# Optimization experiments

Hardware: AMD Instinct MI355X
Metric: run time of the kernel (lower is better)

## Reference

```python
import jax, jax.numpy as jnp
import numpy as np

BS, N, D, H = 4, 128, 768, 8
HD = D // H
FFN = 3072
E = BS * N * N
NORM_FACTOR = 100.0
NORM_CONST = 1.0
EPS_LN = 1e-5


def _ln(v, s, b):
    m = jnp.mean(v, -1, keepdims=True)
    var = jnp.mean(jnp.square(v - m), -1, keepdims=True)
    return (v - m) * jax.lax.rsqrt(var + EPS_LN) * s + b


def _glu(v, w, b):
    a, g = jnp.split(v @ w.T + b, 2, axis=-1)
    return a * jnp.square(jax.nn.relu(g))  # GLU with ReLU^2 gate activation


def setup_inputs() -> dict:
    key = jax.random.key(0)
    ks = jax.random.split(key, 24)
    rn = lambda i, shape, s=1.0: jax.random.normal(ks[i], shape, jnp.float32) * s
    # fully-connected per-graph edge_index with block structure
    base = jnp.arange(BS, dtype=jnp.int32) * N
    ii = jnp.repeat(jnp.arange(N, dtype=jnp.int32), N)
    jj = jnp.tile(jnp.arange(N, dtype=jnp.int32), N)
    row = (base[:, None] + ii[None, :]).reshape(-1)
    col = (base[:, None] + jj[None, :]).reshape(-1)
    edge_index = jnp.stack([row, col], 0)  # [2, E]
    return {
        'h': rn(0, (BS * N, D)),
        'x': rn(1, (BS * N, 3)),
        'edge_attr': rn(2, (E, 1)),
        'node_mask': jnp.ones((BS * N, 1), jnp.float32),
        'edge_mask': jnp.ones((E, 1), jnp.float32),
        'linker_mask': jnp.ones((BS * N, 1), jnp.float32),
        'in_proj_w': rn(3, (3 * D, D), 0.02), 'in_proj_b': jnp.zeros((3 * D,)),
        'out_proj_w': rn(4, (D, D), 0.02), 'out_proj_b': jnp.zeros((D,)),
        'ln1_s': jnp.ones((D,)), 'ln1_b': jnp.zeros((D,)),
        'ln2_s': jnp.ones((D,)), 'ln2_b': jnp.zeros((D,)),
        'fc1_w': rn(5, (2 * FFN, D), 0.02), 'fc1_b': jnp.zeros((2 * FFN,)),
        'fc2_w': rn(6, (2 * D, FFN), 0.02), 'fc2_b': jnp.zeros((2 * D,)),
        'efc1_w': rn(7, (H, 2), 0.5), 'efc1_b': jnp.zeros((H,)),
        'efc2_w': rn(8, (H, 2), 0.5), 'efc2_b': jnp.zeros((H,)),
        'cm1_w': rn(9, (D, 2 * D + 2), 0.02), 'cm1_b': jnp.zeros((D,)),
        'cm2_w': rn(10, (D, D), 0.02), 'cm2_b': jnp.zeros((D,)),
        'cm3_w': rn(11, (1, D), 0.001),
        'edge_index': edge_index,
    }


def _forward(h, x, edge_attr, node_mask, edge_mask, linker_mask,
             in_proj_w, in_proj_b, out_proj_w, out_proj_b,
             ln1_s, ln1_b, ln2_s, ln2_b, fc1_w, fc1_b, fc2_w, fc2_b,
             efc1_w, efc1_b, efc2_w, efc2_b,
             cm1_w, cm1_b, cm2_w, cm2_b, cm3_w, edge_index):
    row, col = edge_index[0], edge_index[1]
    # coord2diff
    diff = x[row] - x[col]                                   # [E,3]
    radial = jnp.sum(jnp.square(diff), 1, keepdims=True)     # [E,1]
    coord_diff = diff / (jnp.sqrt(radial + 1e-8) + NORM_CONST)
    ea = jnp.concatenate([radial, edge_attr], 1)             # [E,2]

    def edge_to_heads(w, b):
        y = (ea @ w.T + b) * edge_mask                       # [E,H]
        return jnp.transpose(y.reshape(BS, N, N, H), (0, 3, 1, 2))  # [BS,H,N,N]

    attn_bias = edge_to_heads(efc1_w, efc1_b)
    gw = edge_to_heads(efc2_w, efc2_b)

    # Graphormer3DEncoderLayer (eval mode: dropout = identity)
    hb = h.reshape(BS, N, D)
    hn = _ln(hb, ln1_s, ln1_b)
    q, k, v = jnp.split(hn @ in_proj_w.T + in_proj_b, 3, axis=-1)
    q = q.reshape(BS, N, H, HD) * (HD ** -0.5)
    k = k.reshape(BS, N, H, HD)
    v = v.reshape(BS, N, H, HD)
    scores = jnp.einsum('bihd,bjhd->bhij', q, k) + attn_bias
    probs = jnp.tanh(gw) * jax.nn.softmax(scores, axis=-1)   # tanh-gated softmax
    att = jnp.einsum('bhij,bjhd->bihd', probs, v).reshape(BS, N, D)
    h1 = hb + (att @ out_proj_w.T + out_proj_b)
    ff = _ln(h1, ln2_s, ln2_b)
    ff = jax.nn.gelu(_glu(ff, fc1_w, fc1_b), approximate=False)
    ff = _glu(ff, fc2_w, fc2_b)
    h_out = (h1 + ff).reshape(BS * N, D) * node_mask

    # EquivariantUpdate (tanh=False branch)
    ei = jnp.concatenate([h_out[row], h_out[col], ea], 1)    # [E, 2D+2]
    t = jax.nn.silu(ei @ cm1_w.T + cm1_b)
    t = jax.nn.silu(t @ cm2_w.T + cm2_b)
    s = t @ cm3_w.T                                          # [E,1]
    trans = coord_diff * s * edge_mask
    agg = jax.ops.segment_sum(trans, row, num_segments=BS * N) / NORM_FACTOR
    x_out = (x + agg * linker_mask) * node_mask
    return h_out, x_out


def reference(h, x, edge_attr, node_mask, edge_mask, linker_mask,
              in_proj_w, in_proj_b, out_proj_w, out_proj_b,
              ln1_s, ln1_b, ln2_s, ln2_b, fc1_w, fc1_b, fc2_w, fc2_b,
              efc1_w, efc1_b, efc2_w, efc2_b,
              cm1_w, cm1_b, cm2_w, cm2_b, cm3_w, edge_index):
    return _forward(h, x, edge_attr, node_mask, edge_mask, linker_mask,
                    in_proj_w, in_proj_b, out_proj_w, out_proj_b,
                    ln1_s, ln1_b, ln2_s, ln2_b, fc1_w, fc1_b, fc2_w, fc2_b,
                    efc1_w, efc1_b, efc2_w, efc2_b,
                    cm1_w, cm1_b, cm2_w, cm2_b, cm3_w, edge_index)
```

## Files before the change

### kernel.cpp

```cpp
#include <hip/hip_runtime.h>
#include <cstdint>
#include <cstddef>

#define BSZ   4
#define NN    128
#define DD    768
#define HH    8
#define HD    96
#define FFN   3072
#define NNODE (BSZ*NN)
#define NE    (NNODE*NN)

typedef unsigned short u16;
typedef __bf16 bf16x8 __attribute__((ext_vector_type(8)));
typedef float  f32x4  __attribute__((ext_vector_type(4)));
typedef unsigned short u16x8 __attribute__((ext_vector_type(8)));
typedef unsigned short u16x4 __attribute__((ext_vector_type(4)));
typedef unsigned short u16x2 __attribute__((ext_vector_type(2)));

__device__ __forceinline__ float bf2f(u16 a){
    unsigned u = ((unsigned)a) << 16; float f; __builtin_memcpy(&f, &u, 4); return f;
}
__device__ __forceinline__ u16 f2bf(float f){
    unsigned u; __builtin_memcpy(&u, &f, 4);
    u = (u + 0x7fffu + ((u >> 16) & 1u)) >> 16;
    return (u16)u;
}
__device__ __forceinline__ f32x4 mfma16(bf16x8 a, bf16x8 b, f32x4 c){
    return __builtin_amdgcn_mfma_f32_16x16x32_bf16(a, b, c, 0, 0, 0);
}
__device__ __forceinline__ bf16x8 frag(const u16* p){
    u16x8 v = *(const u16x8*)p; return __builtin_bit_cast(bf16x8, v);
}
__device__ __forceinline__ void gload16(const void* g, void* l){
    __builtin_amdgcn_global_load_lds((const __attribute__((address_space(1))) void*)g,
                                     (__attribute__((address_space(3))) void*)l, 16, 0, 0);
}
__device__ __forceinline__ float fsilu(float f){
    return f * __builtin_amdgcn_rcpf(1.f + __expf(-f));
}
__device__ __forceinline__ float wred_sum(float v){
    #pragma unroll
    for (int m = 1; m < 64; m <<= 1) v += __shfl_xor(v, m);
    return v;
}
__device__ __forceinline__ float wred_max(float v){
    #pragma unroll
    for (int m = 1; m < 64; m <<= 1) v = fmaxf(v, __shfl_xor(v, m));
    return v;
}

__global__ __launch_bounds__(256) void ln_k(const float* __restrict__ in,
                                            const float* __restrict__ sc,
                                            const float* __restrict__ bi,
                                            u16* __restrict__ out){
    int row = blockIdx.x, tid = threadIdx.x;
    const float* r = in + (size_t)row * DD;
    float x0 = r[tid], x1 = r[tid + 256], x2 = r[tid + 512];
    float s = x0 + x1 + x2, q = x0*x0 + x1*x1 + x2*x2;
    s = wred_sum(s); q = wred_sum(q);
    __shared__ float rs[4], rq[4];
    int w = tid >> 6;
    if ((tid & 63) == 0){ rs[w] = s; rq[w] = q; }
    __syncthreads();
    float ts = rs[0] + rs[1] + rs[2] + rs[3];
    float tq = rq[0] + rq[1] + rq[2] + rq[3];
    float mean = ts * (1.f / DD);
    float var  = tq * (1.f / DD) - mean * mean;
    float rstd = rsqrtf(var + 1e-5f);
    u16* o = out + (size_t)row * DD;
    o[tid]       = f2bf((x0 - mean) * rstd * sc[tid]       + bi[tid]);
    o[tid + 256] = f2bf((x1 - mean) * rstd * sc[tid + 256] + bi[tid + 256]);
    o[tid + 512] = f2bf((x2 - mean) * rstd * sc[tid + 512] + bi[tid + 512]);
}

__device__ __forceinline__ void stage64(u16* __restrict__ dst, const u16* __restrict__ src,
                                        int ld, int kk, int tid){
    #pragma unroll
    for (int p = 0; p < 2; p++){
        int idx = p * 256 + tid;
        int row = idx >> 3, ch = idx & 7;
        int sch = ch ^ (row & 7);
        gload16(src + (size_t)row * ld + kk + sch * 8, dst + idx * 8);
    }
}

__device__ __forceinline__ void stageA(u16* __restrict__ As, const u16* __restrict__ A,
                                       int m0, int lda, int kk, int tid){
    #pragma unroll
    for (int p = 0; p < 2; p++){
        int idx = p * 256 + tid;
        int row = idx >> 3, ch = idx & 7;
        *(uint4*)&As[row * 72 + ch * 8] = *(const uint4*)(A + (size_t)(m0 + row) * lda + kk + ch * 8);
    }
}
__device__ __forceinline__ void stageBf32(u16* __restrict__ Bs, const float* __restrict__ B,
                                          int n0, int ldb, int kk, int tid){
    #pragma unroll
    for (int p = 0; p < 4; p++){
        int idx = p * 256 + tid;
        int row = idx >> 4, c4 = idx & 15;
        float4 v = *(const float4*)(B + (size_t)(n0 + row) * ldb + kk + c4 * 4);
        u16x4 o; o[0] = f2bf(v.x); o[1] = f2bf(v.y); o[2] = f2bf(v.z); o[3] = f2bf(v.w);
        *(u16x4*)&Bs[row * 72 + c4 * 4] = o;
    }
}

#define GEMM_PRO(AB, BB)                                                            \
    const int tid = threadIdx.x;                                                    \
    const int m0 = blockIdx.y * 64, n0 = blockIdx.x * 64;                           \
    const int w = tid >> 6, lane = tid & 63, quad = lane >> 4, l15 = lane & 15;     \
    const int wy = w >> 1, wx = w & 1;                                              \
    const int swz = (l15 & 7) << 4;                                                 \
    const u16* Abase = AB; const u16* Bbase = BB;

__global__ __launch_bounds__(256) void gemm_bt2(const u16* __restrict__ A, int lda,
                                                const u16* __restrict__ B, int ldb,
                                                const float* __restrict__ bias,
                                                u16* __restrict__ C, int ldc, int K){
    __shared__ u16 As[2][64 * 64];
    __shared__ u16 Bs[2][64 * 64];
    GEMM_PRO(A + (size_t)m0 * lda, B + (size_t)n0 * ldb)
    f32x4 acc[2][2];
    #pragma unroll
    for (int i = 0; i < 2; i++)
        #pragma unroll
        for (int j = 0; j < 2; j++){ f32x4 z = {0.f,0.f,0.f,0.f}; acc[i][j] = z; }

    stage64(As[0], Abase, lda, 0, tid);
    stage64(Bs[0], Bbase, ldb, 0, tid);
    __syncthreads();
    const int NS = K / 64;
    #pragma unroll 1
    for (int s = 0; s < NS; s++){
        const int cur = s & 1;
        if (s + 1 < NS){
            stage64(As[cur ^ 1], Abase, lda, (s + 1) * 64, tid);
            stage64(Bs[cur ^ 1], Bbase, ldb, (s + 1) * 64, tid);
        }
        const char* ab = (const char*)&As[cur][0];
        const char* bb = (const char*)&Bs[cur][0];
        #pragma unroll
        for (int k0 = 0; k0 < 64; k0 += 32){
            const int kbx = ((k0 + quad * 8) * 2) ^ swz;
            bf16x8 a0 = frag((const u16*)(ab + (wy * 32 + l15) * 128 + kbx));
            bf16x8 a1 = frag((const u16*)(ab + (wy * 32 + 16 + l15) * 128 + kbx));
            bf16x8 b0 = frag((const u16*)(bb + (wx * 32 + l15) * 128 + kbx));
            bf16x8 b1 = frag((const u16*)(bb + (wx * 32 + 16 + l15) * 128 + kbx));
            acc[0][0] = mfma16(a0, b0, acc[0][0]);
            acc[0][1] = mfma16(a0, b1, acc[0][1]);
            acc[1][0] = mfma16(a1, b0, acc[1][0]);
            acc[1][1] = mfma16(a1, b1, acc[1][1]);
        }
        __syncthreads();
    }
    #pragma unroll
    for (int j = 0; j < 2; j++){
        int n = n0 + wx * 32 + j * 16 + l15;
        float bv = bias[n];
        #pragma unroll
        for (int i = 0; i < 2; i++){
            #pragma unroll
            for (int r = 0; r < 4; r++){
                int m = m0 + wy * 32 + i * 16 + quad * 4 + r;
                C[(size_t)m * ldc + n] = f2bf(acc[i][j][r] + bv);
            }
        }
    }
}

__global__ __launch_bounds__(256) void gemm_proj2(const u16* __restrict__ A,
                                                  const u16* __restrict__ B,
                                                  const float* __restrict__ bias,
                                                  const float* __restrict__ h,
                                                  float* __restrict__ h1f){
    __shared__ u16 As[2][64 * 64];
    __shared__ u16 Bs[2][64 * 64];
    GEMM_PRO(A + (size_t)m0 * DD, B + (size_t)n0 * DD)
    f32x4 acc[2][2];
    #pragma unroll
    for (int i = 0; i < 2; i++)
        #pragma unroll
        for (int j = 0; j < 2; j++){ f32x4 z = {0.f,0.f,0.f,0.f}; acc[i][j] = z; }

    stage64(As[0], Abase, DD, 0, tid);
    stage64(Bs[0], Bbase, DD, 0, tid);
    __syncthreads();
    #pragma unroll 1
    for (int s = 0; s < 12; s++){
        const int cur = s & 1;
        if (s + 1 < 12){
            stage64(As[cur ^ 1], Abase, DD, (s + 1) * 64, tid);
            stage64(Bs[cur ^ 1], Bbase, DD, (s + 1) * 64, tid);
        }
        const char* ab = (const char*)&As[cur][0];
        const char* bb = (const char*)&Bs[cur][0];
        #pragma unroll
        for (int k0 = 0; k0 < 64; k0 += 32){
            const int kbx = ((k0 + quad * 8) * 2) ^ swz;
            bf16x8 a0 = frag((const u16*)(ab + (wy * 32 + l15) * 128 + kbx));
            bf16x8 a1 = frag((const u16*)(ab + (wy * 32 + 16 + l15) * 128 + kbx));
            bf16x8 b0 = frag((const u16*)(bb + (wx * 32 + l15) * 128 + kbx));
            bf16x8 b1 = frag((const u16*)(bb + (wx * 32 + 16 + l15) * 128 + kbx));
            acc[0][0] = mfma16(a0, b0, acc[0][0]);
            acc[0][1] = mfma16(a0, b1, acc[0][1]);
            acc[1][0] = mfma16(a1, b0, acc[1][0]);
            acc[1][1] = mfma16(a1, b1, acc[1][1]);
        }
        __syncthreads();
    }
    #pragma unroll
    for (int j = 0; j < 2; j++){
        int n = n0 + wx * 32 + j * 16 + l15;
        float bv = bias[n];
        #pragma unroll
        for (int i = 0; i < 2; i++){
            #pragma unroll
            for (int r = 0; r < 4; r++){
                int m = m0 + wy * 32 + i * 16 + quad * 4 + r;
                h1f[(size_t)m * DD + n] = acc[i][j][r] + bv + h[(size_t)m * DD + n];
            }
        }
    }
}

template<int MODE>
__global__ __launch_bounds__(256) void gemm_glu2(const u16* __restrict__ A, int lda,
                                                 const u16* __restrict__ B, int ldb,
                                                 const float* __restrict__ bias, int half_off, int K,
                                                 const float* __restrict__ h1f,
                                                 const float* __restrict__ nodemask,
                                                 u16* __restrict__ Cb, int ldc,
                                                 float* __restrict__ Cf){
    __shared__ u16 As[2][64 * 64];
    __shared__ u16 Ba[2][64 * 64];
    __shared__ u16 Bg[2][64 * 64];
    GEMM_PRO(A + (size_t)m0 * lda, B + (size_t)n0 * ldb)
    const u16* Gbase = B + (size_t)(half_off + n0) * ldb;
    f32x4 accA[2][2], accG[2][2];
    #pragma unroll
    for (int i = 0; i < 2; i++)
        #pragma unroll
        for (int j = 0; j < 2; j++){ f32x4 z = {0.f,0.f,0.f,0.f}; accA[i][j] = z; accG[i][j] = z; }

    stage64(As[0], Abase, lda, 0, tid);
    stage64(Ba[0], Bbase, ldb, 0, tid);
    stage64(Bg[0], Gbase, ldb, 0, tid);
    __syncthreads();
    const int NS = K / 64;
    #pragma unroll 1
    for (int s = 0; s < NS; s++){
        const int cur = s & 1;
        if (s + 1 < NS){
            stage64(As[cur ^ 1], Abase, lda, (s + 1) * 64, tid);
            stage64(Ba[cur ^ 1], Bbase, ldb, (s + 1) * 64, tid);
            stage64(Bg[cur ^ 1], Gbase, ldb, (s + 1) * 64, tid);
        }
        const char* ab = (const char*)&As[cur][0];
        const char* bab = (const char*)&Ba[cur][0];
        const char* bgb = (const char*)&Bg[cur][0];
        #pragma unroll
        for (int k0 = 0; k0 < 64; k0 += 32){
            const int kbx = ((k0 + quad * 8) * 2) ^ swz;
            bf16x8 a0  = frag((const u16*)(ab + (wy * 32 + l15) * 128 + kbx));
            bf16x8 a1  = frag((const u16*)(ab + (wy * 32 + 16 + l15) * 128 + kbx));
            bf16x8 ba0 = frag((const u16*)(bab + (wx * 32 + l15) * 128 + kbx));
            bf16x8 ba1 = frag((const u16*)(bab + (wx * 32 + 16 + l15) * 128 + kbx));
            bf16x8 bg0 = frag((const u16*)(bgb + (wx * 32 + l15) * 128 + kbx));
            bf16x8 bg1 = frag((const u16*)(bgb + (wx * 32 + 16 + l15) * 128 + kbx));
            accA[0][0] = mfma16(a0, ba0, accA[0][0]);
            accA[0][1] = mfma16(a0, ba1, accA[0][1]);
            accA[1][0] = mfma16(a1, ba0, accA[1][0]);
            accA[1][1] = mfma16(a1, ba1, accA[1][1]);
            accG[0][0] = mfma16(a0, bg0, accG[0][0]);
            accG[0][1] = mfma16(a0, bg1, accG[0][1]);
            accG[1][0] = mfma16(a1, bg0, accG[1][0]);
            accG[1][1] = mfma16(a1, bg1, accG[1][1]);
        }
        __syncthreads();
    }
    #pragma unroll
    for (int j = 0; j < 2; j++){
        int n = n0 + wx * 32 + j * 16 + l15;
        float bva = bias[n];
        float bvg = bias[half_off + n];
        #pragma unroll
        for (int i = 0; i < 2; i++){
            #pragma unroll
            for (int r = 0; r < 4; r++){
                int m = m0 + wy * 32 + i * 16 + quad * 4 + r;
                float a = accA[i][j][r] + bva;
                float g = accG[i][j][r] + bvg;
                float rg = fmaxf(g, 0.f);
                float t = a * rg * rg;
                if (MODE == 0){
                    float v = 0.5f * t * (1.f + erff(t * 0.70710678118654752f));
                    Cb[(size_t)m * ldc + n] = f2bf(v);
                } else {
                    float v = (t + h1f[(size_t)m * DD + n]) * nodemask[m];
                    Cf[(size_t)m * DD + n] = v;
                    Cb[(size_t)m * DD + n] = f2bf(v);
                }
            }
        }
    }
}

__global__ __launch_bounds__(256) void gemm_pq2(const u16* __restrict__ A,
                                                const u16* __restrict__ Wpq,
                                                const float* __restrict__ bias,
                                                u16* __restrict__ C){
    __shared__ u16 As[2][64 * 64];
    __shared__ u16 Bp[2][64 * 64];
    __shared__ u16 Bq[2][64 * 64];
    GEMM_PRO(A + (size_t)m0 * DD, Wpq + (size_t)n0 * DD)
    const u16* Gbase = Wpq + (size_t)(768 + n0) * DD;
    f32x4 accP[2][2], accQ[2][2];
    #pragma unroll
    for (int i = 0; i < 2; i++)
        #pragma unroll
        for (int j = 0; j < 2; j++){ f32x4 z = {0.f,0.f,0.f,0.f}; accP[i][j] = z; accQ[i][j] = z; }

    stage64(As[0], Abase, DD, 0, tid);
    stage64(Bp[0], Bbase, DD, 0, tid);
    stage64(Bq[0], Gbase, DD, 0, tid);
    __syncthreads();
    #pragma unroll 1
    for (int s = 0; s < 12; s++){
        const int cur = s & 1;
        if (s + 1 < 12){
            stage64(As[cur ^ 1], Abase, DD, (s + 1) * 64, tid);
            stage64(Bp[cur ^ 1], Bbase, DD, (s + 1) * 64, tid);
            stage64(Bq[cur ^ 1], Gbase, DD, (s + 1) * 64, tid);
        }
        const char* ab  = (const char*)&As[cur][0];
        const char* bpb = (const char*)&Bp[cur][0];
        const char* bqb = (const char*)&Bq[cur][0];
        #pragma unroll
        for (int k0 = 0; k0 < 64; k0 += 32){
            const int kbx = ((k0 + quad * 8) * 2) ^ swz;
            bf16x8 a0  = frag((const u16*)(ab + (wy * 32 + l15) * 128 + kbx));
            bf16x8 a1  = frag((const u16*)(ab + (wy * 32 + 16 + l15) * 128 + kbx));
            bf16x8 bp0 = frag((const u16*)(bpb + (wx * 32 + l15) * 128 + kbx));
            bf16x8 bp1 = frag((const u16*)(bpb + (wx * 32 + 16 + l15) * 128 + kbx));
            bf16x8 bq0 = frag((const u16*)(bqb + (wx * 32 + l15) * 128 + kbx));
            bf16x8 bq1 = frag((const u16*)(bqb + (wx * 32 + 16 + l15) * 128 + kbx));
            accP[0][0] = mfma16(a0, bp0, accP[0][0]);
            accP[0][1] = mfma16(a0, bp1, accP[0][1]);
            accP[1][0] = mfma16(a1, bp0, accP[1][0]);
            accP[1][1] = mfma16(a1, bp1, accP[1][1]);
            accQ[0][0] = mfma16(a0, bq0, accQ[0][0]);
            accQ[0][1] = mfma16(a0, bq1, accQ[0][1]);
            accQ[1][0] = mfma16(a1, bq0, accQ[1][0]);
            accQ[1][1] = mfma16(a1, bq1, accQ[1][1]);
        }
        __syncthreads();
    }
    #pragma unroll
    for (int j = 0; j < 2; j++){
        int n = n0 + wx * 32 + j * 16 + l15;
        float bv = bias[n];
        #pragma unroll
        for (int i = 0; i < 2; i++){
            #pragma unroll
            for (int r = 0; r < 4; r++){
                int m = m0 + wy * 32 + i * 16 + quad * 4 + r;
                C[(size_t)m * 1536 + n]       = f2bf(accP[i][j][r] + bv);
                C[(size_t)m * 1536 + 768 + n] = f2bf(accQ[i][j][r]);
            }
        }
    }
}

__global__ void prep2_k(const float* __restrict__ W, u16* __restrict__ O,
                        float* __restrict__ c01){
    int idx = blockIdx.x * 256 + threadIdx.x;
    if (idx < 768){
        c01[idx]       = W[(size_t)idx * 1538 + 1536];
        c01[768 + idx] = W[(size_t)idx * 1538 + 1537];
    }
    if (idx >= 768 * 384) return;
    int n = idx / 384, kp = idx - n * 384, k = kp * 2;
    float2 vp = *(const float2*)(W + (size_t)n * 1538 + k);
    float2 vq = *(const float2*)(W + (size_t)n * 1538 + 768 + k);
    u16x2 op; op[0] = f2bf(vp.x); op[1] = f2bf(vp.y);
    u16x2 oq; oq[0] = f2bf(vq.x); oq[1] = f2bf(vq.y);
    *(u16x2*)&O[(size_t)n * 768 + k]         = op;
    *(u16x2*)&O[(size_t)(768 + n) * 768 + k] = oq;
}

__global__ __launch_bounds__(256) void gemm_bt(const u16* __restrict__ A, int lda,
                                               const float* __restrict__ B, int ldb,
                                               const float* __restrict__ bias,
                                               u16* __restrict__ C, int ldc, int K){
    __shared__ u16 As[64 * 72];
    __shared__ u16 Bs[64 * 72];
    const int tid = threadIdx.x;
    const int m0 = blockIdx.y * 64, n0 = blockIdx.x * 64;
    const int w = tid >> 6, lane = tid & 63, quad = lane >> 4, l15 = lane & 15;
    const int wy = w >> 1, wx = w & 1;
    f32x4 acc[2][2];
    #pragma unroll
    for (int i = 0; i < 2; i++)
        #pragma unroll
        for (int j = 0; j < 2; j++){ f32x4 z = {0.f,0.f,0.f,0.f}; acc[i][j] = z; }

    for (int kk = 0; kk < K; kk += 64){
        stageA(As, A, m0, lda, kk, tid);
        stageBf32(Bs, B, n0, ldb, kk, tid);
        __syncthreads();
        #pragma unroll
        for (int k0 = 0; k0 < 64; k0 += 32){
            int kb = k0 + quad * 8;
            bf16x8 a0 = frag(&As[(wy * 32 + l15) * 72 + kb]);
            bf16x8 a1 = frag(&As[(wy * 32 + 16 + l15) * 72 + kb]);
            bf16x8 b0 = frag(&Bs[(wx * 32 + l15) * 72 + kb]);
            bf16x8 b1 = frag(&Bs[(wx * 32 + 16 + l15) * 72 + kb]);
            acc[0][0] = mfma16(a0, b0, acc[0][0]);
            acc[0][1] = mfma16(a0, b1, acc[0][1]);
            acc[1][0] = mfma16(a1, b0, acc[1][0]);
            acc[1][1] = mfma16(a1, b1, acc[1][1]);
        }
        __syncthreads();
    }
    #pragma unroll
    for (int j = 0; j < 2; j++){
        int n = n0 + wx * 32 + j * 16 + l15;
        float bv = bias[n];
        #pragma unroll
        for (int i = 0; i < 2; i++){
            #pragma unroll
            for (int r = 0; r < 4; r++){
                int m = m0 + wy * 32 + i * 16 + quad * 4 + r;
                C[(size_t)m * ldc + n] = f2bf(acc[i][j][r] + bv);
            }
        }
    }
}

__global__ __launch_bounds__(256) void gemm_proj(const u16* __restrict__ A,
                                                 const float* __restrict__ B,
                                                 const float* __restrict__ bias,
                                                 const float* __restrict__ h,
                                                 float* __restrict__ h1f){
    __shared__ u16 As[64 * 72];
    __shared__ u16 Bs[64 * 72];
    const int tid = threadIdx.x;
    const int m0 = blockIdx.y * 64, n0 = blockIdx.x * 64;
    const int w = tid >> 6, lane = tid & 63, quad = lane >> 4, l15 = lane & 15;
    const int wy = w >> 1, wx = w & 1;
    f32x4 acc[2][2];
    #pragma unroll
    for (int i = 0; i < 2; i++)
        #pragma unroll
        for (int j = 0; j < 2; j++){ f32x4 z = {0.f,0.f,0.f,0.f}; acc[i][j] = z; }

    for (int kk = 0; kk < DD; kk += 64){
        stageA(As, A, m0, DD, kk, tid);
        stageBf32(Bs, B, n0, DD, kk, tid);
        __syncthreads();
        #pragma unroll
        for (int k0 = 0; k0 < 64; k0 += 32){
            int kb = k0 + quad * 8;
            bf16x8 a0 = frag(&As[(wy * 32 + l15) * 72 + kb]);
            bf16x8 a1 = frag(&As[(wy * 32 + 16 + l15) * 72 + kb]);
            bf16x8 b0 = frag(&Bs[(wx * 32 + l15) * 72 + kb]);
            bf16x8 b1 = frag(&Bs[(wx * 32 + 16 + l15) * 72 + kb]);
            acc[0][0] = mfma16(a0, b0, acc[0][0]);
            acc[0][1] = mfma16(a0, b1, acc[0][1]);
            acc[1][0] = mfma16(a1, b0, acc[1][0]);
            acc[1][1] = mfma16(a1, b1, acc[1][1]);
        }
        __syncthreads();
    }
    #pragma unroll
    for (int j = 0; j < 2; j++){
        int n = n0 + wx * 32 + j * 16 + l15;
        float bv = bias[n];
        #pragma unroll
        for (int i = 0; i < 2; i++){
            #pragma unroll
            for (int r = 0; r < 4; r++){
                int m = m0 + wy * 32 + i * 16 + quad * 4 + r;
                h1f[(size_t)m * DD + n] = acc[i][j][r] + bv + h[(size_t)m * DD + n];
            }
        }
    }
}

template<int MODE>
__global__ __launch_bounds__(256) void gemm_glu(const u16* __restrict__ A, int lda,
                                                const float* __restrict__ B, int ldb,
                                                const float* __restrict__ bias, int half_off, int K,
                                                const float* __restrict__ h1f,
                                                const float* __restrict__ nodemask,
                                                u16* __restrict__ Cb, int ldc,
                                                float* __restrict__ Cf){
    __shared__ u16 As[64 * 72];
    __shared__ u16 Ba[64 * 72];
    __shared__ u16 Bg[64 * 72];
    const int tid = threadIdx.x;
    const int m0 = blockIdx.y * 64, n0 = blockIdx.x * 64;
    const int w = tid >> 6, lane = tid & 63, quad = lane >> 4, l15 = lane & 15;
    const int wy = w >> 1, wx = w & 1;
    f32x4 accA[2][2], accG[2][2];
    #pragma unroll
    for (int i = 0; i < 2; i++)
        #pragma unroll
        for (int j = 0; j < 2; j++){ f32x4 z = {0.f,0.f,0.f,0.f}; accA[i][j] = z; accG[i][j] = z; }

    for (int kk = 0; kk < K; kk += 64){
        stageA(As, A, m0, lda, kk, tid);
        stageBf32(Ba, B, n0, ldb, kk, tid);
        stageBf32(Bg, B, half_off + n0, ldb, kk, tid);
        __syncthreads();
        #pragma unroll
        for (int k0 = 0; k0 < 64; k0 += 32){
            int kb = k0 + quad * 8;
            bf16x8 a0  = frag(&As[(wy * 32 + l15) * 72 + kb]);
            bf16x8 a1  = frag(&As[(wy * 32 + 16 + l15) * 72 + kb]);
            bf16x8 ba0 = frag(&Ba[(wx * 32 + l15) * 72 + kb]);
            bf16x8 ba1 = frag(&Ba[(wx * 32 + 16 + l15) * 72 + kb]);
            bf16x8 bg0 = frag(&Bg[(wx * 32 + l15) * 72 + kb]);
            bf16x8 bg1 = frag(&Bg[(wx * 32 + 16 + l15) * 72 + kb]);
            accA[0][0] = mfma16(a0, ba0, accA[0][0]);
            accA[0][1] = mfma16(a0, ba1, accA[0][1]);
            accA[1][0] = mfma16(a1, ba0, accA[1][0]);
            accA[1][1] = mfma16(a1, ba1, accA[1][1]);
            accG[0][0] = mfma16(a0, bg0, accG[0][0]);
            accG[0][1] = mfma16(a0, bg1, accG[0][1]);
            accG[1][0] = mfma16(a1, bg0, accG[1][0]);
            accG[1][1] = mfma16(a1, bg1, accG[1][1]);
        }
        __syncthreads();
    }
    #pragma unroll
    for (int j = 0; j < 2; j++){
        int n = n0 + wx * 32 + j * 16 + l15;
        float bva = bias[n];
        float bvg = bias[half_off + n];
        #pragma unroll
        for (int i = 0; i < 2; i++){
            #pragma unroll
            for (int r = 0; r < 4; r++){
                int m = m0 + wy * 32 + i * 16 + quad * 4 + r;
                float a = accA[i][j][r] + bva;
                float g = accG[i][j][r] + bvg;
                float rg = fmaxf(g, 0.f);
                float t = a * rg * rg;
                if (MODE == 0){
                    float v = 0.5f * t * (1.f + erff(t * 0.70710678118654752f));
                    Cb[(size_t)m * ldc + n] = f2bf(v);
                } else {
                    float v = (t + h1f[(size_t)m * DD + n]) * nodemask[m];
                    Cf[(size_t)m * DD + n] = v;
                    Cb[(size_t)m * DD + n] = f2bf(v);
                }
            }
        }
    }
}

__global__ __launch_bounds__(256) void gemm_pq(const u16* __restrict__ A,
                                               const float* __restrict__ W,
                                               const float* __restrict__ bias,
                                               u16* __restrict__ C){
    __shared__ u16 As[64 * 72];
    __shared__ u16 Bp[64 * 72];
    __shared__ u16 Bq[64 * 72];
    const int tid = threadIdx.x;
    const int m0 = blockIdx.y * 64, n0 = blockIdx.x * 64;
    const int w = tid >> 6, lane = tid & 63, quad = lane >> 4, l15 = lane & 15;
    const int wy = w >> 1, wx = w & 1;
    f32x4 accP[2][2], accQ[2][2];
    #pragma unroll
    for (int i = 0; i < 2; i++)
        #pragma unroll
        for (int j = 0; j < 2; j++){ f32x4 z = {0.f,0.f,0.f,0.f}; accP[i][j] = z; accQ[i][j] = z; }

    for (int kk = 0; kk < DD; kk += 64){
        stageA(As, A, m0, DD, kk, tid);
        #pragma unroll
        for (int p = 0; p < 8; p++){
            int idx = p * 256 + tid;
            int row = idx >> 5, c2 = idx & 31;
            size_t base = (size_t)(n0 + row) * 1538 + kk + c2 * 2;
            float2 vp = *(const float2*)(W + base);
            float2 vq = *(const float2*)(W + base + 768);
            u16x2 op; op[0] = f2bf(vp.x); op[1] = f2bf(vp.y);
            u16x2 oq; oq[0] = f2bf(vq.x); oq[1] = f2bf(vq.y);
            *(u16x2*)&Bp[row * 72 + c2 * 2] = op;
            *(u16x2*)&Bq[row * 72 + c2 * 2] = oq;
        }
        __syncthreads();
        #pragma unroll
        for (int k0 = 0; k0 < 64; k0 += 32){
            int kb = k0 + quad * 8;
            bf16x8 a0  = frag(&As[(wy * 32 + l15) * 72 + kb]);
            bf16x8 a1  = frag(&As[(wy * 32 + 16 + l15) * 72 + kb]);
            bf16x8 bp0 = frag(&Bp[(wx * 32 + l15) * 72 + kb]);
            bf16x8 bp1 = frag(&Bp[(wx * 32 + 16 + l15) * 72 + kb]);
            bf16x8 bq0 = frag(&Bq[(wx * 32 + l15) * 72 + kb]);
            bf16x8 bq1 = frag(&Bq[(wx * 32 + 16 + l15) * 72 + kb]);
            accP[0][0] = mfma16(a0, bp0, accP[0][0]);
            accP[0][1] = mfma16(a0, bp1, accP[0][1]);
            accP[1][0] = mfma16(a1, bp0, accP[1][0]);
            accP[1][1] = mfma16(a1, bp1, accP[1][1]);
            accQ[0][0] = mfma16(a0, bq0, accQ[0][0]);
            accQ[0][1] = mfma16(a0, bq1, accQ[0][1]);
            accQ[1][0] = mfma16(a1, bq0, accQ[1][0]);
            accQ[1][1] = mfma16(a1, bq1, accQ[1][1]);
        }
        __syncthreads();
    }
    #pragma unroll
    for (int j = 0; j < 2; j++){
        int n = n0 + wx * 32 + j * 16 + l15;
        float bv = bias[n];
        #pragma unroll
        for (int i = 0; i < 2; i++){
            #pragma unroll
            for (int r = 0; r < 4; r++){
                int m = m0 + wy * 32 + i * 16 + quad * 4 + r;
                C[(size_t)m * 1536 + n]       = f2bf(accP[i][j][r] + bv);
                C[(size_t)m * 1536 + 768 + n] = f2bf(accQ[i][j][r]);
            }
        }
    }
}

#define KSTR 104
__global__ __launch_bounds__(128) void attn_k(const u16* __restrict__ qkv,
                                              const float* __restrict__ x,
                                              const float* __restrict__ eattr,
                                              const float* __restrict__ emask,
                                              const float* __restrict__ e1w, const float* __restrict__ e1b,
                                              const float* __restrict__ e2w, const float* __restrict__ e2b,
                                              u16* __restrict__ att){
    __shared__ u16 Ks[NN * KSTR];
    __shared__ u16 Vs[NN * KSTR];
    __shared__ float xs[NN * 3];
    __shared__ float qs[HD];
    __shared__ float ps[NN];
    __shared__ float red[2];
    const int tid = threadIdx.x;
    const int h = blockIdx.y, b = blockIdx.z;
    const int i0 = blockIdx.x * 16;

    for (int idx = tid; idx < NN * 12; idx += 128){
        int j = idx / 12, c = idx - j * 12;
        const u16* base = qkv + (size_t)(b * NN + j) * 2304 + h * HD + c * 8;
        *(u16x8*)&Ks[j * KSTR + c * 8] = *(const u16x8*)(base + DD);
        *(u16x8*)&Vs[j * KSTR + c * 8] = *(const u16x8*)(base + 1536);
    }
    if (tid < NN){
        xs[tid * 3]     = x[(b * NN + tid) * 3];
        xs[tid * 3 + 1] = x[(b * NN + tid) * 3 + 1];
        xs[tid * 3 + 2] = x[(b * NN + tid) * 3 + 2];
    }
    __syncthreads();
    const float w1r = e1w[h * 2], w1a = e1w[h * 2 + 1], b1 = e1b[h];
    const float w2r = e2w[h * 2], w2a = e2w[h * 2 + 1], b2v = e2b[h];
    const int wv = tid >> 6;

    for (int ig = 0; ig < 16; ig++){
        const int i = i0 + ig, ni = b * NN + i;
        if (tid < HD) qs[tid] = bf2f(qkv[(size_t)ni * 2304 + h * HD + tid]) * 0.10206207261596577f;
        __syncthreads();
        const int j = tid;
        float s = 0.f;
        #pragma unroll
        for (int c = 0; c < 12; c++){
            u16x8 kv = *(const u16x8*)&Ks[j * KSTR + c * 8];
            #pragma unroll
            for (int t = 0; t < 8; t++) s += qs[c * 8 + t] * bf2f(kv[t]);
        }
        float d0 = xs[i * 3]     - xs[j * 3];
        float d1 = xs[i * 3 + 1] - xs[j * 3 + 1];
        float d2 = xs[i * 3 + 2] - xs[j * 3 + 2];
        float radial = d0*d0 + d1*d1 + d2*d2;
        int e = ni * NN + j;
        float at = eattr[e], em = emask[e];
        s += (w1r * radial + w1a * at + b1) * em;
        float gw = (w2r * radial + w2a * at + b2v) * em;
        float m1 = wred_max(s);
        if ((tid & 63) == 0) red[wv] = m1;
        __syncthreads();
        float M = fmaxf(red[0], red[1]);
        __syncthreads();
        float ev = __expf(s - M);
        float s1 = wred_sum(ev);
        if ((tid & 63) == 0) red[wv] = s1;
        __syncthreads();
        float S = red[0] + red[1];
        ps[j] = tanhf(gw) * ev / S;
        __syncthreads();
        if (tid < HD){
            float a = 0.f;
            #pragma unroll 8
            for (int jj = 0; jj < NN; jj++) a += ps[jj] * bf2f(Vs[jj * KSTR + tid]);
            att[(size_t)ni * DD + h * HD + tid] = f2bf(a);
        }
        __syncthreads();
    }
}

__global__ void prep_k(const float* __restrict__ cm1w, float* __restrict__ c01){
    int idx = blockIdx.x * 256 + threadIdx.x;
    if (idx < 768){
        c01[idx]       = cm1w[(size_t)idx * 1538 + 1536];
        c01[768 + idx] = cm1w[(size_t)idx * 1538 + 1537];
    }
}

__global__ void w2bf_k(const float* __restrict__ W, u16* __restrict__ O, int n){
    int i4 = (blockIdx.x * 256 + threadIdx.x) * 4;
    if (i4 < n){
        float4 v = *(const float4*)(W + i4);
        u16x4 o; o[0] = f2bf(v.x); o[1] = f2bf(v.y); o[2] = f2bf(v.z); o[3] = f2bf(v.w);
        *(u16x4*)&O[i4] = o;
    }
}

__global__ void w2bf5_k(const float* __restrict__ a0, u16* __restrict__ o0, int s0,
                        const float* __restrict__ a1, u16* __restrict__ o1, int s1,
                        const float* __restrict__ a2, u16* __restrict__ o2, int s2,
                        const float* __restrict__ a3, u16* __restrict__ o3, int s3,
                        const float* __restrict__ a4, u16* __restrict__ o4, int s4){
    int off = (blockIdx.x * 256 + threadIdx.x) * 4;
    const float* s; u16* d;
    if (off < s0){ s = a0; d = o0; }
    else { off -= s0;
    if (off < s1){ s = a1; d = o1; }
    else { off -= s1;
    if (off < s2){ s = a2; d = o2; }
    else { off -= s2;
    if (off < s3){ s = a3; d = o3; }
    else { off -= s3;
    if (off >= s4) return; s = a4; d = o4; }}}}
    float4 v = *(const float4*)(s + off);
    u16x4 o; o[0] = f2bf(v.x); o[1] = f2bf(v.y); o[2] = f2bf(v.z); o[3] = f2bf(v.w);
    *(u16x4*)&d[off] = o;
}

__global__ __launch_bounds__(256) void t1_k(const u16* __restrict__ PQ,
                                            const float* __restrict__ c01,
                                            const float* __restrict__ x,
                                            const float* __restrict__ eattr,
                                            u16* __restrict__ T1g){
    int cid = blockIdx.x * 256 + threadIdx.x;
    int e = cid / 96;
    int kc = cid - e * 96;
    int k = kc * 8;
    int r = e >> 7;
    int j = e & 127;
    int b = r >> 7;
    int nc = b * NN + j;
    float d0 = x[r * 3]     - x[nc * 3];
    float d1 = x[r * 3 + 1] - x[nc * 3 + 1];
    float d2 = x[r * 3 + 2] - x[nc * 3 + 2];
    float rad = d0 * d0 + d1 * d1 + d2 * d2;
    float at = eattr[e];
    u16x8 pv = *(const u16x8*)(PQ + (size_t)r  * 1536 + k);
    u16x8 qv = *(const u16x8*)(PQ + (size_t)nc * 1536 + 768 + k);
    float4 c0a = *(const float4*)(c01 + k);
    float4 c0b = *(const float4*)(c01 + k + 4);
    float4 c1a = *(const float4*)(c01 + 768 + k);
    float4 c1b = *(const float4*)(c01 + 768 + k + 4);
    float c0r[8] = {c0a.x,c0a.y,c0a.z,c0a.w,c0b.x,c0b.y,c0b.z,c0b.w};
    float c1r[8] = {c1a.x,c1a.y,c1a.z,c1a.w,c1b.x,c1b.y,c1b.z,c1b.w};
    u16x8 ov;
    #pragma unroll
    for (int t = 0; t < 8; t++){
        float f = bf2f(pv[t]) + bf2f(qv[t]) + rad * c0r[t] + at * c1r[t];
        ov[t] = f2bf(fsilu(f));
    }
    *(u16x8*)&T1g[(size_t)e * 768 + k] = ov;
}

__global__ __launch_bounds__(1024, 1) void edge_k(const u16* __restrict__ T1g,
                                                  const u16* __restrict__ W2b,
                                                  const float* __restrict__ b2,
                                                  const float* __restrict__ w3,
                                                  const float* __restrict__ x,
                                                  const float* __restrict__ emask,
                                                  float* __restrict__ aggpart){
    __shared__ u16 Bd[2][384 * 64];
    __shared__ u16 T1d[2][128 * 64];
    __shared__ float sacc[128];
    __shared__ float red6[6];
    const int tid = threadIdx.x;
    const int r = blockIdx.x;
    const int b = r >> 7;

    if (tid < 128) sacc[tid] = 0.f;

    auto stageB = [&](int np, int kk, int p){
        #pragma unroll
        for (int c = 0; c < 3; c++){
            int idx = c * 1024 + tid;
            int row = idx >> 3, ch = idx & 7;
            int sch = ch ^ (row & 7);
            gload16(W2b + (size_t)(np * 384 + row) * 768 + kk + sch * 8, &Bd[p][idx * 8]);
        }
    };
    auto stageT1 = [&](int kk, int p){
        int idx = tid;
        int row = idx >> 3, ch = idx & 7;
        int sch = ch ^ (row & 7);
        gload16(T1g + (size_t)(r * NN + row) * 768 + kk + sch * 8, &T1d[p][idx * 8]);
    };

    const int w = tid >> 6, lane = tid & 63, quad = lane >> 4, l15 = lane & 15;
    const int wr = w >> 3, wc = w & 7;
    const int swz = (l15 & 7) << 4;
    f32x4 acc[4][3];

    stageB(0, 0, 0);
    stageT1(0, 0);
    __syncthreads();

    #pragma unroll 1
    for (int np = 0; np < 2; np++){
        #pragma unroll
        for (int i = 0; i < 4; i++)
            #pragma unroll
            for (int jj = 0; jj < 3; jj++){ f32x4 z = {0.f,0.f,0.f,0.f}; acc[i][jj] = z; }

        #pragma unroll 1
        for (int kk64 = 0; kk64 < 12; kk64++){
            const int cur = kk64 & 1;
            const int s  = np * 12 + kk64;
            const int ns = s + 1;
            const int nkk = (kk64 == 11) ? 0 : kk64 + 1;
            const int nnp = (kk64 == 11) ? np + 1 : np;
            if (ns < 24){
                stageB(nnp, nkk * 64, nkk & 1);
                stageT1(nkk * 64, nkk & 1);
            }
            const char* tb = (const char*)&T1d[cur][0];
            const char* bb = (const char*)&Bd[cur][0];
            #pragma unroll
            for (int k0 = 0; k0 < 64; k0 += 32){
                const int kbx = ((k0 + quad * 8) * 2) ^ swz;
                bf16x8 aF[4], bF[3];
                #pragma unroll
                for (int i = 0; i < 4; i++)
                    aF[i] = frag((const u16*)(tb + (wr * 64 + i * 16 + l15) * 128 + kbx));
                #pragma unroll
                for (int jj = 0; jj < 3; jj++)
                    bF[jj] = frag((const u16*)(bb + (wc * 48 + jj * 16 + l15) * 128 + kbx));
                #pragma unroll
                for (int i = 0; i < 4; i++)
                    #pragma unroll
                    for (int jj = 0; jj < 3; jj++)
                        acc[i][jj] = mfma16(aF[i], bF[jj], acc[i][jj]);
            }
            __syncthreads();
        }

        float part[4][4];
        #pragma unroll
        for (int i = 0; i < 4; i++)
            #pragma unroll
            for (int rr = 0; rr < 4; rr++) part[i][rr] = 0.f;
        #pragma unroll
        for (int jj = 0; jj < 3; jj++){
            int n = np * 384 + wc * 48 + jj * 16 + l15;
            float bb2 = b2[n], cc = w3[n];
            #pragma unroll
            for (int i = 0; i < 4; i++)
                #pragma unroll
                for (int rr = 0; rr < 4; rr++){
                    float v = fsilu(acc[i][jj][rr] + bb2);
                    part[i][rr] += v * cc;
                }
        }
        #pragma unroll
        for (int i = 0; i < 4; i++)
            #pragma unroll
            for (int rr = 0; rr < 4; rr++){
                float v = part[i][rr];
                v += __shfl_xor(v, 1); v += __shfl_xor(v, 2);
                v += __shfl_xor(v, 4); v += __shfl_xor(v, 8);
                if (l15 == 0) atomicAdd(&sacc[wr * 64 + i * 16 + quad * 4 + rr], v);
            }
    }
    __syncthreads();
    if (tid < 128){
        const float xr0 = x[r * 3], xr1 = x[r * 3 + 1], xr2 = x[r * 3 + 2];
        int nc = b * NN + tid;
        float d0 = xr0 - x[nc * 3], d1 = xr1 - x[nc * 3 + 1], d2 = xr2 - x[nc * 3 + 2];
        float radial = d0 * d0 + d1 * d1 + d2 * d2;
        float inv = 1.f / (sqrtf(radial + 1e-8f) + 1.f);
        float sv = sacc[tid] * emask[r * NN + tid];
        float tx = d0 * inv * sv, ty = d1 * inv * sv, tz = d2 * inv * sv;
        #pragma unroll
        for (int m = 1; m < 64; m <<= 1){
            tx += __shfl_xor(tx, m); ty += __shfl_xor(ty, m); tz += __shfl_xor(tz, m);
        }
        if (lane == 0){
            red6[w * 3 + 0] = tx; red6[w * 3 + 1] = ty; red6[w * 3 + 2] = tz;
        }
    }
    __syncthreads();
    if (tid == 0){
        aggpart[r * 3 + 0] = red6[0] + red6[3];
        aggpart[r * 3 + 1] = red6[1] + red6[4];
        aggpart[r * 3 + 2] = red6[2] + red6[5];
    }
}

__global__ __launch_bounds__(512) void edge_fb_k(const u16* __restrict__ PQ,
                                                 const u16* __restrict__ W2b,
                                                 const float* __restrict__ b2,
                                                 const float* __restrict__ w3,
                                                 const float* __restrict__ c01,
                                                 const float* __restrict__ x,
                                                 const float* __restrict__ eattr,
                                                 const float* __restrict__ emask,
                                                 float* __restrict__ aggpart){
    __shared__ u16 Bd[2][192 * 64];
    __shared__ u16 T1s[128 * 64];
    __shared__ float sacc[128];
    __shared__ float red6[6];
    const int tid = threadIdx.x;
    const int r = blockIdx.x;
    const int b = r >> 7;

    const float xr0 = x[r * 3], xr1 = x[r * 3 + 1], xr2 = x[r * 3 + 2];
    const int jl0 = tid >> 3, jl1 = 64 + jl0;
    float rad0, eat0, rad1, eat1;
    {
        int nc0 = b * NN + jl0;
        float d0 = xr0 - x[nc0 * 3], d1 = xr1 - x[nc0 * 3 + 1], d2 = xr2 - x[nc0 * 3 + 2];
        rad0 = d0 * d0 + d1 * d1 + d2 * d2;
        eat0 = eattr[r * NN + jl0];
        int nc1 = b * NN + jl1;
        float e0 = xr0 - x[nc1 * 3], e1 = xr1 - x[nc1 * 3 + 1], e2 = xr2 - x[nc1 * 3 + 2];
        rad1 = e0 * e0 + e1 * e1 + e2 * e2;
        eat1 = eattr[r * NN + jl1];
    }
    if (tid < 128) sacc[tid] = 0.f;

    auto stageB = [&](int np, int kk, int p){
        #pragma unroll
        for (int c = 0; c < 3; c++){
            int idx = c * 512 + tid;
            int row = idx >> 3, ch = idx & 7;
            int sch = ch ^ (row & 7);
            gload16(W2b + (size_t)(np * 192 + row) * 768 + kk + sch * 8, &Bd[p][idx * 8]);
        }
    };
    auto stageT1 = [&](int kk){
        const int kc = tid & 7, k = kc * 8;
        float4 c0a = *(const float4*)(c01 + kk + k);
        float4 c0b = *(const float4*)(c01 + kk + k + 4);
        float4 c1a = *(const float4*)(c01 + 768 + kk + k);
        float4 c1b = *(const float4*)(c01 + 768 + kk + k + 4);
        float c0r[8] = {c0a.x,c0a.y,c0a.z,c0a.w,c0b.x,c0b.y,c0b.z,c0b.w};
        float c1r[8] = {c1a.x,c1a.y,c1a.z,c1a.w,c1b.x,c1b.y,c1b.z,c1b.w};
        u16x8 pv = *(const u16x8*)(PQ + (size_t)r * 1536 + kk + k);
        #pragma unroll
        for (int c = 0; c < 2; c++){
            int jl = c ? jl1 : jl0;
            float rj = c ? rad1 : rad0;
            float aj = c ? eat1 : eat0;
            int nc = b * NN + jl;
            u16x8 qv = *(const u16x8*)(PQ + (size_t)nc * 1536 + 768 + kk + k);
            u16x8 ov;
            #pragma unroll
            for (int t = 0; t < 8; t++){
                float f = bf2f(pv[t]) + bf2f(qv[t]) + rj * c0r[t] + aj * c1r[t];
                ov[t] = f2bf(fsilu(f));
            }
            *(u16x8*)&T1s[jl * 64 + ((kc ^ (jl & 7)) * 8)] = ov;
        }
    };

    const int w = tid >> 6, lane = tid & 63, quad = lane >> 4, l15 = lane & 15;
    const int wr = w >> 1, wc = w & 1;
    const int swz = (l15 & 7) << 4;
    f32x4 acc[2][6];

    stageB(0, 0, 0);
    stageT1(0);
    __syncthreads();

    #pragma unroll 1
    for (int np = 0; np < 4; np++){
        #pragma unroll
        for (int i = 0; i < 2; i++)
            #pragma unroll
            for (int jj = 0; jj < 6; jj++){ f32x4 z = {0.f,0.f,0.f,0.f}; acc[i][jj] = z; }

        #pragma unroll 1
        for (int kk64 = 0; kk64 < 12; kk64++){
            const int cur = kk64 & 1;
            const int s  = np * 12 + kk64;
            const int ns = s + 1;
            const int nkk = (kk64 == 11) ? 0 : kk64 + 1;
            const int nnp = (kk64 == 11) ? np + 1 : np;
            if (ns < 48) stageB(nnp, nkk * 64, nkk & 1);
            const char* tb = (const char*)&T1s[0];
            const char* bb = (const char*)&Bd[cur][0];
            #pragma unroll
            for (int k0 = 0; k0 < 64; k0 += 32){
                const int kbx = ((k0 + quad * 8) * 2) ^ swz;
                bf16x8 a0 = frag((const u16*)(tb + (wr * 32 + l15) * 128 + kbx));
                bf16x8 a1 = frag((const u16*)(tb + (wr * 32 + 16 + l15) * 128 + kbx));
                #pragma unroll
                for (int jj = 0; jj < 6; jj++){
                    bf16x8 bF = frag((const u16*)(bb + (wc * 96 + jj * 16 + l15) * 128 + kbx));
                    acc[0][jj] = mfma16(a0, bF, acc[0][jj]);
                    acc[1][jj] = mfma16(a1, bF, acc[1][jj]);
                }
            }
            __syncthreads();
            if (ns < 48) stageT1(nkk * 64);
            __syncthreads();
        }

        float part[2][4];
        #pragma unroll
        for (int i = 0; i < 2; i++)
            #pragma unroll
            for (int rr = 0; rr < 4; rr++) part[i][rr] = 0.f;
        #pragma unroll
        for (int jj = 0; jj < 6; jj++){
            int n = np * 192 + wc * 96 + jj * 16 + l15;
            float bb2 = b2[n], cc = w3[n];
            #pragma unroll
            for (int i = 0; i < 2; i++)
                #pragma unroll
                for (int rr = 0; rr < 4; rr++){
                    float v = fsilu(acc[i][jj][rr] + bb2);
                    part[i][rr] += v * cc;
                }
        }
        #pragma unroll
        for (int i = 0; i < 2; i++)
            #pragma unroll
            for (int rr = 0; rr < 4; rr++){
                float v = part[i][rr];
                v += __shfl_xor(v, 1); v += __shfl_xor(v, 2);
                v += __shfl_xor(v, 4); v += __shfl_xor(v, 8);
                if (l15 == 0) atomicAdd(&sacc[wr * 32 + i * 16 + quad * 4 + rr], v);
            }
    }
    __syncthreads();
    if (tid < 128){
        int nc = b * NN + tid;
        float d0 = xr0 - x[nc * 3], d1 = xr1 - x[nc * 3 + 1], d2 = xr2 - x[nc * 3 + 2];
        float radial = d0 * d0 + d1 * d1 + d2 * d2;
        float inv = 1.f / (sqrtf(radial + 1e-8f) + 1.f);
        float sv = sacc[tid] * emask[r * NN + tid];
        float tx = d0 * inv * sv, ty = d1 * inv * sv, tz = d2 * inv * sv;
        #pragma unroll
        for (int m = 1; m < 64; m <<= 1){
            tx += __shfl_xor(tx, m); ty += __shfl_xor(ty, m); tz += __shfl_xor(tz, m);
        }
        if (lane == 0){
            red6[w * 3 + 0] = tx; red6[w * 3 + 1] = ty; red6[w * 3 + 2] = tz;
        }
    }
    __syncthreads();
    if (tid == 0){
        aggpart[r * 3 + 0] = red6[0] + red6[3];
        aggpart[r * 3 + 1] = red6[1] + red6[4];
        aggpart[r * 3 + 2] = red6[2] + red6[5];
    }
}

__global__ void xout_k(const float* __restrict__ x, const float* __restrict__ linker,
                       const float* __restrict__ nodemask, const float* __restrict__ aggpart,
                       float* __restrict__ out){
    int idx = blockIdx.x * 256 + threadIdx.x;
    if (idx >= NNODE * 3) return;
    int node = idx / 3, c = idx - node * 3;
    float s = aggpart[node * 3 + c];
    out[(size_t)NNODE * DD + idx] = (x[idx] + s * 0.01f * linker[node]) * nodemask[node];
}

extern "C" void kernel_launch(void* const* d_in, const int* in_sizes, int n_in,
                              void* d_out, int out_size, void* d_ws, size_t ws_size,
                              hipStream_t stream){
    (void)in_sizes; (void)n_in; (void)out_size;
    const float* h        = (const float*)d_in[0];
    const float* x        = (const float*)d_in[1];
    const float* eattr    = (const float*)d_in[2];
    const float* nodemask = (const float*)d_in[3];
    const float* emask    = (const float*)d_in[4];
    const float* linker   = (const float*)d_in[5];
    const float* in_w  = (const float*)d_in[6];  const float* in_b  = (const float*)d_in[7];
    const float* out_w = (const float*)d_in[8];  const float* out_b = (const float*)d_in[9];
    const float* ln1s  = (const float*)d_in[10]; const float* ln1b  = (const float*)d_in[11];
    const float* ln2s  = (const float*)d_in[12]; const float* ln2b  = (const float*)d_in[13];
    const float* fc1w  = (const float*)d_in[14]; const float* fc1b  = (const float*)d_in[15];
    const float* fc2w  = (const float*)d_in[16]; const float* fc2b  = (const float*)d_in[17];
    const float* e1w   = (const float*)d_in[18]; const float* e1b   = (const float*)d_in[19];
    const float* e2w   = (const float*)d_in[20]; const float* e2b   = (const float*)d_in[21];
    const float* cm1w  = (const float*)d_in[22]; const float* cm1b  = (const float*)d_in[23];
    const float* cm2w  = (const float*)d_in[24]; const float* cm2b  = (const float*)d_in[25];
    const float* cm3w  = (const float*)d_in[26];
    float* out = (float*)d_out;

    char* ws = (char*)d_ws;
    u16*   hn      = (u16*)  (ws + 0);
    u16*   qkv     = (u16*)  (ws + 786432);
    u16*   att     = (u16*)  (ws + 3145728);
    float* h1f     = (float*)(ws + 0);
    u16*   ffin    = (u16*)  (ws + 1572864);
    u16*   g1      = (u16*)  (ws + 2359296);
    u16*   houtb   = (u16*)  (ws + 5505024);
    u16*   PQ      = (u16*)  (ws + 0);
    float* c01     = (float*)(ws + 1572864);
    float* aggpart = (float*)(ws + 1579008);
    u16*   cm2b16  = (u16*)  (ws + 6291456);
    u16*   in_wb   = (u16*)  (ws + 8388608);
    u16*   out_wb  = (u16*)  (ws + 11927552);
    u16*   fc1b16  = (u16*)  (ws + 13107200);
    u16*   fc2b16  = (u16*)  (ws + 22544384);
    u16*   wpq     = (u16*)  (ws + 22544384);
    u16*   T1g     = (u16*)  (ws + 8388608);
    const bool fast = ws_size >= (size_t)8388608 + (size_t)100663296;

    if (fast){
        w2bf5_k <<<12096, 256, 0, stream>>>(in_w,  in_wb,  2304*768,
                                            out_w, out_wb, 768*768,
                                            fc1w,  fc1b16, 6144*768,
                                            fc2w,  fc2b16, 1536*3072,
                                            cm2w,  cm2b16, 768*768);
    } else {
        w2bf_k <<<576, 256, 0, stream>>>(cm2w, cm2b16, DD*DD);
    }
    ln_k       <<<NNODE, 256, 0, stream>>>(h, ln1s, ln1b, hn);
    if (fast){
        gemm_bt2    <<<dim3(2304/64, NNODE/64), 256, 0, stream>>>(hn, DD, in_wb, DD, in_b, qkv, 2304, DD);
        attn_k      <<<dim3(NN/16, HH, BSZ), 128, 0, stream>>>(qkv, x, eattr, emask, e1w, e1b, e2w, e2b, att);
        gemm_proj2  <<<dim3(DD/64, NNODE/64), 256, 0, stream>>>(att, out_wb, out_b, h, h1f);
        ln_k        <<<NNODE, 256, 0, stream>>>(h1f, ln2s, ln2b, ffin);
        gemm_glu2<0><<<dim3(FFN/64, NNODE/64), 256, 0, stream>>>(ffin, DD, fc1b16, DD, fc1b, FFN, DD,
                                                                 nullptr, nullptr, g1, FFN, nullptr);
        gemm_glu2<1><<<dim3(DD/64, NNODE/64), 256, 0, stream>>>(g1, FFN, fc2b16, FFN, fc2b, DD, FFN,
                                                                h1f, nodemask, houtb, DD, out);
        prep2_k     <<<1152, 256, 0, stream>>>(cm1w, wpq, c01);
        gemm_pq2    <<<dim3(DD/64, NNODE/64), 256, 0, stream>>>(houtb, wpq, cm1b, PQ);
        t1_k        <<<24576, 256, 0, stream>>>(PQ, c01, x, eattr, T1g);
        edge_k      <<<512, 1024, 0, stream>>>(T1g, cm2b16, cm2b, cm3w, x, emask, aggpart);
    } else {
        gemm_bt    <<<dim3(2304/64, NNODE/64), 256, 0, stream>>>(hn, DD, in_w, DD, in_b, qkv, 2304, DD);
        attn_k     <<<dim3(NN/16, HH, BSZ), 128, 0, stream>>>(qkv, x, eattr, emask, e1w, e1b, e2w, e2b, att);
        gemm_proj  <<<dim3(DD/64, NNODE/64), 256, 0, stream>>>(att, out_w, out_b, h, h1f);
        ln_k       <<<NNODE, 256, 0, stream>>>(h1f, ln2s, ln2b, ffin);
        gemm_glu<0><<<dim3(FFN/64, NNODE/64), 256, 0, stream>>>(ffin, DD, fc1w, DD, fc1b, FFN, DD,
                                                                nullptr, nullptr, g1, FFN, nullptr);
        gemm_glu<1><<<dim3(DD/64, NNODE/64), 256, 0, stream>>>(g1, FFN, fc2w, FFN, fc2b, DD, FFN,
                                                               h1f, nodemask, houtb, DD, out);
        prep_k     <<<3, 256, 0, stream>>>(cm1w, c01);
        gemm_pq    <<<dim3(DD/64, NNODE/64), 256, 0, stream>>>(houtb, cm1w, cm1b, PQ);
        edge_fb_k  <<<512, 512, 0, stream>>>(PQ, cm2b16, cm2b, cm3w, c01, x, eattr, emask, aggpart);
    }
    xout_k     <<<6, 256, 0, stream>>>(x, linker, nodemask, aggpart, out);
}
```

Measured before the change: 413.6 us.

## Split-K the fc2 GLU GEMM into four slices with a separate reduction kernel

Replaces the fc2 GLU GEMM, which launched only 96 blocks over K=3072, with a split-K version that launches 384 blocks, each covering a 768-wide K slice and writing fp32 partials. A new reduction kernel sums the four partials, adds the bias, applies the ReLU^2 GLU gate and residual with the node mask, and writes both the fp32 output and the bf16 copy. This is meant to fill more of the GPU's compute units for this small-M GEMM. The cost is an extra launch plus about 12 MB of fp32 partial traffic in workspace.

```diff
diff --git a/kernel.cpp b/kernel.cpp
--- a/kernel.cpp
+++ b/kernel.cpp
@@ -303,6 +303,97 @@
                 }
             }
         }
+    }
+}
+
+__global__ __launch_bounds__(256) void gemm_glu2ks(const u16* __restrict__ A,
+                                                   const u16* __restrict__ B,
+                                                   float* __restrict__ part){
+    __shared__ u16 As[2][64 * 64];
+    __shared__ u16 Ba[2][64 * 64];
+    __shared__ u16 Bg[2][64 * 64];
+    GEMM_PRO(A + (size_t)m0 * FFN, B + (size_t)n0 * FFN)
+    const u16* Gbase = B + (size_t)(DD + n0) * FFN;
+    const int kb0 = blockIdx.z * 768;
+    f32x4 accA[2][2], accG[2][2];
+    #pragma unroll
+    for (int i = 0; i < 2; i++)
+        #pragma unroll
+        for (int j = 0; j < 2; j++){ f32x4 z = {0.f,0.f,0.f,0.f}; accA[i][j] = z; accG[i][j] = z; }
+
+    stage64(As[0], Abase, FFN, kb0, tid);
+    stage64(Ba[0], Bbase, FFN, kb0, tid);
+    stage64(Bg[0], Gbase, FFN, kb0, tid);
+    __syncthreads();
+    #pragma unroll 1
+    for (int s = 0; s < 12; s++){
+        const int cur = s & 1;
+        if (s + 1 < 12){
+            stage64(As[cur ^ 1], Abase, FFN, kb0 + (s + 1) * 64, tid);
+            stage64(Ba[cur ^ 1], Bbase, FFN, kb0 + (s + 1) * 64, tid);
+            stage64(Bg[cur ^ 1], Gbase, FFN, kb0 + (s + 1) * 64, tid);
+        }
+        const char* ab = (const char*)&As[cur][0];
+        const char* bab = (const char*)&Ba[cur][0];
+        const char* bgb = (const char*)&Bg[cur][0];
+        #pragma unroll
+        for (int k0 = 0; k0 < 64; k0 += 32){
+            const int kbx = ((k0 + quad * 8) * 2) ^ swz;
+            bf16x8 a0  = frag((const u16*)(ab + (wy * 32 + l15) * 128 + kbx));
+            bf16x8 a1  = frag((const u16*)(ab + (wy * 32 + 16 + l15) * 128 + kbx));
+            bf16x8 ba0 = frag((const u16*)(bab + (wx * 32 + l15) * 128 + kbx));
+            bf16x8 ba1 = frag((const u16*)(bab + (wx * 32 + 16 + l15) * 128 + kbx));
+            bf16x8 bg0 = frag((const u16*)(bgb + (wx * 32 + l15) * 128 + kbx));
+            bf16x8 bg1 = frag((const u16*)(bgb + (wx * 32 + 16 + l15) * 128 + kbx));
+            accA[0][0] = mfma16(a0, ba0, accA[0][0]);
+            accA[0][1] = mfma16(a0, ba1, accA[0][1]);
+            accA[1][0] = mfma16(a1, ba0, accA[1][0]);
+            accA[1][1] = mfma16(a1, ba1, accA[1][1]);
+            accG[0][0] = mfma16(a0, bg0, accG[0][0]);
+            accG[0][1] = mfma16(a0, bg1, accG[0][1]);
+            accG[1][0] = mfma16(a1, bg0, accG[1][0]);
+            accG[1][1] = mfma16(a1, bg1, accG[1][1]);
+        }
+        __syncthreads();
+    }
+    float* pz = part + (size_t)blockIdx.z * 512 * 1536;
+    #pragma unroll
+    for (int j = 0; j < 2; j++){
+        int n = n0 + wx * 32 + j * 16 + l15;
+        #pragma unroll
+        for (int i = 0; i < 2; i++){
+            #pragma unroll
+            for (int r = 0; r < 4; r++){
+                int m = m0 + wy * 32 + i * 16 + quad * 4 + r;
+                pz[(size_t)m * 1536 + n]       = accA[i][j][r];
+                pz[(size_t)m * 1536 + 768 + n] = accG[i][j][r];
+            }
+        }
+    }
+}
+
+__global__ __launch_bounds__(256) void glu_red_k(const float* __restrict__ part,
+                                                 const float* __restrict__ bias,
+                                                 const float* __restrict__ h1f,
+                                                 const float* __restrict__ nodemask,
+                                                 u16* __restrict__ houtb,
+                                                 float* __restrict__ out){
+    const int m = blockIdx.x, tid = threadIdx.x;
+    const float mask = nodemask[m];
+    #pragma unroll
+    for (int c = tid; c < 768; c += 256){
+        float a = bias[c], g = bias[768 + c];
+        #pragma unroll
+        for (int s = 0; s < 4; s++){
+            const float* pz = part + (size_t)s * 512 * 1536 + (size_t)m * 1536;
+            a += pz[c];
+            g += pz[768 + c];
+        }
+        float rg = fmaxf(g, 0.f);
+        float t = a * rg * rg;
+        float v = (t + h1f[(size_t)m * DD + c]) * mask;
+        out[(size_t)m * DD + c] = v;
+        houtb[(size_t)m * DD + c] = f2bf(v);
     }
 }
 
@@ -1122,6 +1213,7 @@
     u16*   fc1b16  = (u16*)  (ws + 13107200);
     u16*   fc2b16  = (u16*)  (ws + 22544384);
     u16*   wpq     = (u16*)  (ws + 22544384);
+    float* glupart = (float*)(ws + 33554432);
     u16*   T1g     = (u16*)  (ws + 8388608);
     const bool fast = ws_size >= (size_t)8388608 + (size_t)100663296;
 
@@ -1142,8 +1234,8 @@
         ln_k        <<<NNODE, 256, 0, stream>>>(h1f, ln2s, ln2b, ffin);
         gemm_glu2<0><<<dim3(FFN/64, NNODE/64), 256, 0, stream>>>(ffin, DD, fc1b16, DD, fc1b, FFN, DD,
                                                                  nullptr, nullptr, g1, FFN, nullptr);
-        gemm_glu2<1><<<dim3(DD/64, NNODE/64), 256, 0, stream>>>(g1, FFN, fc2b16, FFN, fc2b, DD, FFN,
-                                                                h1f, nodemask, houtb, DD, out);
+        gemm_glu2ks <<<dim3(DD/64, NNODE/64, 4), 256, 0, stream>>>(g1, fc2b16, glupart);
+        glu_red_k   <<<NNODE, 256, 0, stream>>>(glupart, fc2b, h1f, nodemask, houtb, out);
         prep2_k     <<<1152, 256, 0, stream>>>(cm1w, wpq, c01);
         gemm_pq2    <<<dim3(DD/64, NNODE/64), 256, 0, stream>>>(houtb, wpq, cm1b, PQ);
         t1_k        <<<24576, 256, 0, stream>>>(PQ, c01, x, eattr, T1g);
```

Result: faster. 390.7 us (-5.5%).
